# Performance work log

Hardware: AMD Instinct MI355X
Metric: run time of the kernel (lower is better)

## Reference

```python
import jax, jax.numpy as jnp
import numpy as np

# config constants (from init_kwargs)
IMG_W = 800
IMG_H = 320
NUM_POINTS = 72
N_STRIPS = NUM_POINTS - 1
MAX_LANES = 4
REFINE_LAYERS = 3
CLS_W, REG_W, IOU_W = 2.0, 0.5, 2.0
ALPHA_NEG, ALPHA_POS, GAMMA = 0.1, 0.9, 2.0
LIOU_LEN = 15.0


def setup_inputs() -> dict:
    key = jax.random.key(0)
    k1, k2, k3, k4 = jax.random.split(key, 4)
    S, B, N, L, D = REFINE_LAYERS, 32, 2000, MAX_LANES, 2 + 4 + NUM_POINTS
    pred_fir = jax.random.uniform(k1, (S, B, N, D), dtype=jnp.float32)
    pred_sec = jax.random.uniform(k2, (S, B, N, D), dtype=jnp.float32)
    gt = jax.random.uniform(k3, (B, L, D), dtype=jnp.float32)
    gt = gt.at[..., 1].set(1.0)                    # all lanes valid
    # target offsets live in pixel coords; let some fall outside [0, IMG_W) to exercise invalid mask
    gt = gt.at[..., 6:].set(gt[..., 6:] * (IMG_W * 1.1) - 0.05 * IMG_W)
    diff = jax.random.uniform(k4, (S, N), dtype=jnp.float32)
    return {"predictions_fir": pred_fir, "predictions_sec": pred_sec,
            "gt_lane": gt, "diff": diff}


def _greedy_assign(cost):
    # cost: [N, L] -> matched prior row per target column, greedy without replacement
    N = cost.shape[0]
    def body(used, col):
        c = jnp.where(used, jnp.inf, col)
        r = jnp.argmin(c)
        return used.at[r].set(True), r
    _, rows = jax.lax.scan(body, jnp.zeros((N,), bool), cost.T)
    return rows  # [L] int32


def _assign_all(preds, gt):
    # preds: [S,B,N,D], gt: [B,L,D]; matching is under no_grad in the original
    p = jax.lax.stop_gradient(preds)
    t = jax.lax.stop_gradient(gt)
    score = jax.nn.softmax(p[..., :2], axis=-1)[..., 1]            # [S,B,N]
    geo = jnp.abs(p[..., :, None, 2:6] - t[None, :, None, :, 2:6]).sum(-1)   # [S,B,N,L]
    off = jnp.abs(p[..., :, None, 6:] - t[None, :, None, :, 6:] / (IMG_W - 1)).mean(-1)
    cost = geo + off - score[..., None]                            # [S,B,N,L]
    S, B, N, L = cost.shape
    rows = jax.vmap(_greedy_assign)(cost.reshape(S * B, N, L))
    return rows.reshape(S, B, L)


def _smooth_l1(d):
    ad = jnp.abs(d)
    return jnp.where(ad < 1.0, 0.5 * d * d, ad - 0.5)


def _branch_loss(preds, gt):
    # preds: [S,B,N,D], gt: [B,L,D] -> instance loss [N], last matched rows [L]
    S, B, N, _ = preds.shape
    L = gt.shape[1]
    rows = _assign_all(preds, gt)                                  # [S,B,L]

    # focal cls loss, per prior, summed over stages & batch
    cls_t = jax.nn.one_hot(rows, N, dtype=preds.dtype).sum(2)      # [S,B,N] 0/1
    logp = jax.nn.log_softmax(preds[..., :2], axis=-1)
    logpt = jnp.where(cls_t > 0, logp[..., 1], logp[..., 0])
    pt = jnp.exp(logpt)
    alpha_t = jnp.where(cls_t > 0, ALPHA_POS, ALPHA_NEG)
    cls_loss = (-alpha_t * (1.0 - pt) ** GAMMA * logpt).sum((0, 1)) / (B * REFINE_LAYERS)  # [N]

    # gather matched priors: [S,B,L,D]
    pm = jnp.take_along_axis(preds, rows[..., None], axis=2)
    tgt = gt[None]                                                 # [1,B,L,D]

    # smooth-L1 on (y, x, theta, length)
    sc = jnp.array([N_STRIPS, IMG_W - 1, 180.0, N_STRIPS], preds.dtype)
    d = pm[..., 2:6] * sc - tgt[..., 2:6] * sc
    reg_loss = (_smooth_l1(d).mean(-1) / L).sum((0, 1)) / (B * REFINE_LAYERS)  # [L]

    # line IoU loss on offsets
    rp = pm[..., 6:] * (IMG_W - 1)
    rt = jnp.broadcast_to(tgt[..., 6:], rp.shape)
    invalid = (rt < 0) | (rt >= IMG_W)
    ovr = jnp.minimum(rp + LIOU_LEN, rt + LIOU_LEN) - jnp.maximum(rp - LIOU_LEN, rt - LIOU_LEN)
    uni = jnp.maximum(rp + LIOU_LEN, rt + LIOU_LEN) - jnp.minimum(rp - LIOU_LEN, rt - LIOU_LEN)
    ovr = jnp.where(invalid, 0.0, ovr)
    uni = jnp.where(invalid, 0.0, uni)
    iou = ovr.sum(-1) / (uni.sum(-1) + 1e-9)                       # [S,B,L]
    iou_loss = ((1.0 - iou) / L).sum((0, 1)) / (B * REFINE_LAYERS) # [L]

    inst = cls_loss * CLS_W
    rows_last = rows[-1, -1]                                       # last stage, last image
    inst = inst.at[rows_last].add(reg_loss * REG_W + iou_loss * IOU_W)
    return inst


def reference(predictions_fir, predictions_sec, gt_lane, diff):
    loss_A = _branch_loss(predictions_fir, gt_lane)   # [N]
    loss_B = _branch_loss(predictions_sec, gt_lane)   # [N]
    diff_mean = diff.mean(0)                          # [N]
    delta = jax.lax.stop_gradient(jnp.median(loss_A - loss_B))
    loss_A = loss_A - delta / 2
    loss_B = loss_B + delta / 2
    total = jnp.sum((1.0 - diff_mean) * loss_A + diff_mean * loss_B)
    return total
```

## Files before the change

kernel.cpp:

```cpp
#include <hip/hip_runtime.h>
#include <math.h>

#define SDIM 3
#define BDIM 32
#define NPRI 2000
#define LDIM 4
#define DDIM 78
#define NOFF 72
#define NSB (SDIM * BDIM)
#define CHUNK 64
#define NCHUNK 32


__global__ __launch_bounds__(256) void cost_kernel(
    const float* __restrict__ predsA, const float* __restrict__ predsB,
    const float* __restrict__ gt,
    float* __restrict__ costws, float* __restrict__ clsSum)
{
    const int chunk = blockIdx.x;
    const int sb = blockIdx.y;
    const int branch = blockIdx.z;
    const float* preds = branch ? predsB : predsA;
    const int bimg = sb % BDIM;
    const int tid = threadIdx.x;
    const int base_n = chunk * CHUNK;
    const int ntile = min(CHUNK, NPRI - base_n);

    __shared__ float tile[CHUNK * DDIM];
    __shared__ float tg[36 * 8];
    __shared__ float geo4[16];

    {
        const float4* src = (const float4*)(preds + ((size_t)sb * NPRI + base_n) * DDIM);
        const int nf4 = ntile * DDIM / 4;
        for (int k = tid; k < nf4; k += 256) {
            __builtin_amdgcn_global_load_lds(
                (const __attribute__((address_space(1))) unsigned int*)(src + k),
                (__attribute__((address_space(3))) unsigned int*)(&tile[k * 4]),
                16, 0, 0);
        }
    }
    {
        const float* gtb = gt + (size_t)bimg * LDIM * DDIM;
        if (tid < 288) {
            int jj = tid >> 3, t = tid & 7, l = t >> 1, k = t & 1;
            tg[tid] = gtb[l * DDIM + 6 + 2 * jj + k] / 799.0f;
        }
        if (tid < 16) geo4[tid] = gtb[(tid >> 2) * DDIM + 2 + (tid & 3)];
    }
    __syncthreads();

    const int wv = tid >> 6, lane = tid & 63;
    const int il = wv * 16 + (lane >> 2);
    const int h = lane & 3;
    if (il >= ntile) return;
    const int n = base_n + il;
    const float* p = &tile[il * DDIM];

    float offs0 = 0.f, offs1 = 0.f, offs2 = 0.f, offs3 = 0.f;
    const int jj0 = h * 9;
#pragma unroll 3
    for (int jj = jj0; jj < jj0 + 9; ++jj) {
        float pv0 = p[6 + 2 * jj];
        float pv1 = p[7 + 2 * jj];
        const float4* t4 = (const float4*)(tg + jj * 8);
        float4 ta = t4[0], tb = t4[1];
        offs0 += fabsf(pv0 - ta.x); offs0 += fabsf(pv1 - ta.y);
        offs1 += fabsf(pv0 - ta.z); offs1 += fabsf(pv1 - ta.w);
        offs2 += fabsf(pv0 - tb.x); offs2 += fabsf(pv1 - tb.y);
        offs3 += fabsf(pv0 - tb.z); offs3 += fabsf(pv1 - tb.w);
    }
    offs0 += __shfl_xor(offs0, 1); offs1 += __shfl_xor(offs1, 1);
    offs2 += __shfl_xor(offs2, 1); offs3 += __shfl_xor(offs3, 1);
    offs0 += __shfl_xor(offs0, 2); offs1 += __shfl_xor(offs1, 2);
    offs2 += __shfl_xor(offs2, 2); offs3 += __shfl_xor(offs3, 2);

    float a = p[0], b1 = p[1];
    float m = fmaxf(a, b1);
    float ea = expf(a - m), eb = expf(b1 - m);
    float score = eb / (ea + eb);
    float g0 = p[2], g1 = p[3], g2 = p[4], g3 = p[5];

    float mo01 = (h & 1) ? offs1 : offs0;
    float mo23 = (h & 1) ? offs3 : offs2;
    float myoffs = (h & 2) ? mo23 : mo01;

    float geo = fabsf(g0 - geo4[h * 4 + 0]) + fabsf(g1 - geo4[h * 4 + 1])
              + fabsf(g2 - geo4[h * 4 + 2]) + fabsf(g3 - geo4[h * 4 + 3]);
    float* cw = costws + ((size_t)(branch * NSB + sb) * LDIM) * NPRI;
    cw[(size_t)h * NPRI + n] = geo + myoffs / 72.0f - score;

    if (h == 0) {
        float lse = m + logf(ea + eb);
        float logpt = a - lse;
        float pt = expf(logpt);
        float om = 1.0f - pt;
        atomicAdd(&clsSum[branch * NPRI + n], -(0.1f * om * om * logpt));
    }
}

__global__ __launch_bounds__(256) void assignloss_kernel(
    const float* __restrict__ predsA, const float* __restrict__ predsB,
    const float* __restrict__ gt, const float* __restrict__ costws,
    int* __restrict__ rowsws, float* __restrict__ regacc,
    float* __restrict__ corrws)
{
    const int sb = blockIdx.x, branch = blockIdx.y;
    const float* preds = branch ? predsB : predsA;
    const int tid = threadIdx.x;
    const int wv = tid >> 6, lane = tid & 63;
    const int bimg = sb % BDIM;

    __shared__ float cost[LDIM][NPRI];
    __shared__ float redv[4];
    __shared__ int   redi[4];
    __shared__ int   rows_lds[LDIM];

    const float4* src = (const float4*)(costws + (size_t)(branch * NSB + sb) * LDIM * NPRI);
    float4* dst = (float4*)&cost[0][0];
    for (int k = tid; k < LDIM * NPRI / 4; k += 256) dst[k] = src[k];
    __syncthreads();

    for (int l = 0; l < LDIM; ++l) {
        float bv = INFINITY; int bi = 0x7fffffff;
        for (int k = tid; k < NPRI; k += 256) {
            float v = cost[l][k];
            if (v < bv) { bv = v; bi = k; }
        }
#pragma unroll
        for (int off = 32; off > 0; off >>= 1) {
            float v2 = __shfl_down(bv, off);
            int   i2 = __shfl_down(bi, off);
            if (v2 < bv || (v2 == bv && i2 < bi)) { bv = v2; bi = i2; }
        }
        if (lane == 0) { redv[wv] = bv; redi[wv] = bi; }
        __syncthreads();
        if (tid == 0) {
            float fv = redv[0]; int fi = redi[0];
#pragma unroll
            for (int w = 1; w < 4; ++w)
                if (redv[w] < fv || (redv[w] == fv && redi[w] < fi)) { fv = redv[w]; fi = redi[w]; }
            rows_lds[l] = fi;
            cost[0][fi] = INFINITY; cost[1][fi] = INFINITY;
            cost[2][fi] = INFINITY; cost[3][fi] = INFINITY;
        }
        __syncthreads();
    }
    if (tid < LDIM && sb == NSB - 1) rowsws[branch * LDIM + tid] = rows_lds[tid];

    const int l = wv;
    const int row = rows_lds[l];
    const float* pm = preds + ((size_t)sb * NPRI + row) * DDIM;
    const float* tg = gt + ((size_t)bimg * LDIM + l) * DDIM;

    float osum = 0.f, usum = 0.f, rterm = 0.f;
    {
        float rp = pm[6 + lane] * 799.0f;
        float rt = tg[6 + lane];
        bool inv = (rt < 0.0f) || (rt >= 800.0f);
        float ov = fminf(rp, rt) - fmaxf(rp, rt) + 30.0f;
        float un = fmaxf(rp, rt) - fminf(rp, rt) + 30.0f;
        if (!inv) { osum += ov; usum += un; }
    }
    if (lane < 8) {
        float rp = pm[6 + lane + 64] * 799.0f;
        float rt = tg[6 + lane + 64];
        bool inv = (rt < 0.0f) || (rt >= 800.0f);
        float ov = fminf(rp, rt) - fmaxf(rp, rt) + 30.0f;
        float un = fmaxf(rp, rt) - fminf(rp, rt) + 30.0f;
        if (!inv) { osum += ov; usum += un; }
    }
    if (lane < 4) {
        const float scv[4] = {71.0f, 799.0f, 180.0f, 71.0f};
        float s = scv[lane];
        float d = pm[2 + lane] * s - tg[2 + lane] * s;
        float ad = fabsf(d);
        rterm = (ad < 1.0f) ? 0.5f * d * d : ad - 0.5f;
    }
#pragma unroll
    for (int off = 32; off > 0; off >>= 1) {
        osum += __shfl_down(osum, off);
        usum += __shfl_down(usum, off);
        rterm += __shfl_down(rterm, off);
    }
    if (lane == 0) {
        float iou = osum / (usum + 1e-9f);
        atomicAdd(&regacc[branch * 8 + l], (rterm / 4.0f) / 4.0f);
        atomicAdd(&regacc[branch * 8 + 4 + l], (1.0f - iou) / 4.0f);

        float a = pm[0], b1 = pm[1];
        float m = fmaxf(a, b1);
        float ea = expf(a - m), eb = expf(b1 - m);
        float lse = m + logf(ea + eb);
        float lp0 = a - lse, lp1 = b1 - lse;
        float pt0 = expf(lp0), pt1 = expf(lp1);
        float om0 = 1.0f - pt0, om1 = 1.0f - pt1;
        float neg = -(0.1f * om0 * om0 * lp0);
        float pos = -(0.9f * om1 * om1 * lp1);
        atomicAdd(&corrws[branch * NPRI + row], pos - neg);
    }
}

__global__ __launch_bounds__(1024) void final_kernel(
    const float* __restrict__ clsSum, const float* __restrict__ corrws,
    const float* __restrict__ regacc, const int* __restrict__ rowsws,
    const float* __restrict__ diff, float* __restrict__ out)
{
    __shared__ float instA[NPRI];
    __shared__ float instB[NPRI];
    __shared__ float sbuf[2048];
    __shared__ float red[1024];
    const int tid = threadIdx.x;

    for (int n = tid; n < NPRI; n += 1024) {
        float ia = (clsSum[n] + corrws[n]) * (2.0f / 96.0f);
        float ib = (clsSum[NPRI + n] + corrws[NPRI + n]) * (2.0f / 96.0f);
#pragma unroll
        for (int l = 0; l < 4; ++l) {
            if (rowsws[l] == n)
                ia += (regacc[l] / 96.0f) * 0.5f + (regacc[4 + l] / 96.0f) * 2.0f;
            if (rowsws[4 + l] == n)
                ib += (regacc[8 + l] / 96.0f) * 0.5f + (regacc[12 + l] / 96.0f) * 2.0f;
        }
        instA[n] = ia; instB[n] = ib;
        sbuf[n] = ia - ib;
    }
    if (tid < 2048 - NPRI) sbuf[NPRI + tid] = INFINITY;
    __syncthreads();

    for (int k = 2; k <= 2048; k <<= 1) {
        for (int j = k >> 1; j > 0; j >>= 1) {
            for (int i = tid; i < 2048; i += 1024) {
                int ixj = i ^ j;
                if (ixj > i) {
                    bool up = ((i & k) == 0);
                    float x = sbuf[i], y = sbuf[ixj];
                    if ((x > y) == up) { sbuf[i] = y; sbuf[ixj] = x; }
                }
            }
            __syncthreads();
        }
    }
    float delta = 0.5f * (sbuf[999] + sbuf[1000]);

    float acc = 0.0f;
    for (int n = tid; n < NPRI; n += 1024) {
        float dm = (diff[n] + diff[NPRI + n] + diff[2 * NPRI + n]) / 3.0f;
        acc += (1.0f - dm) * (instA[n] - 0.5f * delta)
             + dm * (instB[n] + 0.5f * delta);
    }
    red[tid] = acc;
    __syncthreads();
    for (int s = 512; s > 0; s >>= 1) {
        if (tid < s) red[tid] += red[tid + s];
        __syncthreads();
    }
    if (tid == 0) out[0] = red[0];
}

extern "C" void kernel_launch(void* const* d_in, const int* in_sizes, int n_in,
                              void* d_out, int out_size, void* d_ws, size_t ws_size,
                              hipStream_t stream)
{
    const float* predsA = (const float*)d_in[0];
    const float* predsB = (const float*)d_in[1];
    const float* gt     = (const float*)d_in[2];
    const float* diff   = (const float*)d_in[3];
    float* out = (float*)d_out;

    float* costws = (float*)d_ws;
    int*   rowsws = (int*)(costws + 2 * NSB * LDIM * NPRI);
    float* clsSum = (float*)(rowsws + 8);
    float* corrws = clsSum + 2 * NPRI;
    float* regacc = corrws + 2 * NPRI;

    hipMemsetAsync(clsSum, 0, (4 * NPRI + 16) * sizeof(float), stream);

    dim3 g1(NCHUNK, NSB, 2);
    cost_kernel<<<g1, 256, 0, stream>>>(predsA, predsB, gt, costws, clsSum);

    dim3 g2(NSB, 2);
    assignloss_kernel<<<g2, 256, 0, stream>>>(predsA, predsB, gt, costws,
                                              rowsws, regacc, corrws);

    final_kernel<<<1, 1024, 0, stream>>>(clsSum, corrws, regacc, rowsws, diff, out);
}
```

Measured before the change: 187.0 us.

## Fuse cost computation and greedy assignment into one kernel keeping cost in LDS

Merges the cost kernel and the assignment/loss kernel into a single 1024-thread block per (stage-image, branch). The cost matrix is built directly in shared memory instead of being written to and reread from a global workspace, and one launch is removed. Predictions are now read straight from global memory with per-thread strided float2 loads instead of async LDS staging. Grid parallelism drops from thousands of blocks to 192, which risks underusing the GPU on a bandwidth-bound read.

New measurement: 187.3 us. No clear change (+0.1%).

```diff
diff --git a/kernel.cpp b/kernel.cpp
--- a/kernel.cpp
+++ b/kernel.cpp
@@ -6,40 +6,28 @@
 #define NPRI 2000
 #define LDIM 4
 #define DDIM 78
-#define NOFF 72
 #define NSB (SDIM * BDIM)
-#define CHUNK 64
-#define NCHUNK 32
-
-
-__global__ __launch_bounds__(256) void cost_kernel(
+
+
+__global__ __launch_bounds__(1024) void fused_kernel(
     const float* __restrict__ predsA, const float* __restrict__ predsB,
     const float* __restrict__ gt,
-    float* __restrict__ costws, float* __restrict__ clsSum)
+    int* __restrict__ rowsws, float* __restrict__ regacc,
+    float* __restrict__ corrws, float* __restrict__ clsSum)
 {
-    const int chunk = blockIdx.x;
-    const int sb = blockIdx.y;
-    const int branch = blockIdx.z;
+    const int sb = blockIdx.x, branch = blockIdx.y;
     const float* preds = branch ? predsB : predsA;
     const int bimg = sb % BDIM;
     const int tid = threadIdx.x;
-    const int base_n = chunk * CHUNK;
-    const int ntile = min(CHUNK, NPRI - base_n);
-
-    __shared__ float tile[CHUNK * DDIM];
+    const int wv = tid >> 6, lane = tid & 63;
+
+    __shared__ float cost[LDIM][NPRI];
     __shared__ float tg[36 * 8];
     __shared__ float geo4[16];
-
-    {
-        const float4* src = (const float4*)(preds + ((size_t)sb * NPRI + base_n) * DDIM);
-        const int nf4 = ntile * DDIM / 4;
-        for (int k = tid; k < nf4; k += 256) {
-            __builtin_amdgcn_global_load_lds(
-                (const __attribute__((address_space(1))) unsigned int*)(src + k),
-                (__attribute__((address_space(3))) unsigned int*)(&tile[k * 4]),
-                16, 0, 0);
-        }
-    }
+    __shared__ float redv[16];
+    __shared__ int   redi[16];
+    __shared__ int   rows_lds[LDIM];
+
     {
         const float* gtb = gt + (size_t)bimg * LDIM * DDIM;
         if (tid < 288) {
@@ -50,80 +38,66 @@
     }
     __syncthreads();
 
-    const int wv = tid >> 6, lane = tid & 63;
-    const int il = wv * 16 + (lane >> 2);
-    const int h = lane & 3;
-    if (il >= ntile) return;
-    const int n = base_n + il;
-    const float* p = &tile[il * DDIM];
-
-    float offs0 = 0.f, offs1 = 0.f, offs2 = 0.f, offs3 = 0.f;
-    const int jj0 = h * 9;
-#pragma unroll 3
-    for (int jj = jj0; jj < jj0 + 9; ++jj) {
-        float pv0 = p[6 + 2 * jj];
-        float pv1 = p[7 + 2 * jj];
-        const float4* t4 = (const float4*)(tg + jj * 8);
-        float4 ta = t4[0], tb = t4[1];
-        offs0 += fabsf(pv0 - ta.x); offs0 += fabsf(pv1 - ta.y);
-        offs1 += fabsf(pv0 - ta.z); offs1 += fabsf(pv1 - ta.w);
-        offs2 += fabsf(pv0 - tb.x); offs2 += fabsf(pv1 - tb.y);
-        offs3 += fabsf(pv0 - tb.z); offs3 += fabsf(pv1 - tb.w);
-    }
-    offs0 += __shfl_xor(offs0, 1); offs1 += __shfl_xor(offs1, 1);
-    offs2 += __shfl_xor(offs2, 1); offs3 += __shfl_xor(offs3, 1);
-    offs0 += __shfl_xor(offs0, 2); offs1 += __shfl_xor(offs1, 2);
-    offs2 += __shfl_xor(offs2, 2); offs3 += __shfl_xor(offs3, 2);
-
-    float a = p[0], b1 = p[1];
-    float m = fmaxf(a, b1);
-    float ea = expf(a - m), eb = expf(b1 - m);
-    float score = eb / (ea + eb);
-    float g0 = p[2], g1 = p[3], g2 = p[4], g3 = p[5];
-
-    float mo01 = (h & 1) ? offs1 : offs0;
-    float mo23 = (h & 1) ? offs3 : offs2;
-    float myoffs = (h & 2) ? mo23 : mo01;
-
-    float geo = fabsf(g0 - geo4[h * 4 + 0]) + fabsf(g1 - geo4[h * 4 + 1])
-              + fabsf(g2 - geo4[h * 4 + 2]) + fabsf(g3 - geo4[h * 4 + 3]);
-    float* cw = costws + ((size_t)(branch * NSB + sb) * LDIM) * NPRI;
-    cw[(size_t)h * NPRI + n] = geo + myoffs / 72.0f - score;
-
-    if (h == 0) {
-        float lse = m + logf(ea + eb);
-        float logpt = a - lse;
-        float pt = expf(logpt);
-        float om = 1.0f - pt;
-        atomicAdd(&clsSum[branch * NPRI + n], -(0.1f * om * om * logpt));
-    }
-}
-
-__global__ __launch_bounds__(256) void assignloss_kernel(
-    const float* __restrict__ predsA, const float* __restrict__ predsB,
-    const float* __restrict__ gt, const float* __restrict__ costws,
-    int* __restrict__ rowsws, float* __restrict__ regacc,
-    float* __restrict__ corrws)
-{
-    const int sb = blockIdx.x, branch = blockIdx.y;
-    const float* preds = branch ? predsB : predsA;
-    const int tid = threadIdx.x;
-    const int wv = tid >> 6, lane = tid & 63;
-    const int bimg = sb % BDIM;
-
-    __shared__ float cost[LDIM][NPRI];
-    __shared__ float redv[4];
-    __shared__ int   redi[4];
-    __shared__ int   rows_lds[LDIM];
-
-    const float4* src = (const float4*)(costws + (size_t)(branch * NSB + sb) * LDIM * NPRI);
-    float4* dst = (float4*)&cost[0][0];
-    for (int k = tid; k < LDIM * NPRI / 4; k += 256) dst[k] = src[k];
+    const int h = tid & 3;
+    const float* gpb = preds + (size_t)sb * NPRI * DDIM;
+
+    for (int pass = 0; pass < 8; ++pass) {
+        const int n = pass * 256 + (tid >> 2);
+        if (n < NPRI) {
+            const float* p = gpb + (size_t)n * DDIM;
+            float2 hd0 = *(const float2*)(p);
+            float2 hd1 = *(const float2*)(p + 2);
+            float2 hd2 = *(const float2*)(p + 4);
+            const float2* pb = (const float2*)(p + 6 + h * 18);
+            float2 ov[9];
+#pragma unroll
+            for (int q = 0; q < 9; ++q) ov[q] = pb[q];
+
+            float offs0 = 0.f, offs1 = 0.f, offs2 = 0.f, offs3 = 0.f;
+#pragma unroll
+            for (int q = 0; q < 9; ++q) {
+                float pv0 = ov[q].x;
+                float pv1 = ov[q].y;
+                const float4* t4 = (const float4*)(tg + (h * 9 + q) * 8);
+                float4 ta = t4[0], tb = t4[1];
+                offs0 += fabsf(pv0 - ta.x); offs0 += fabsf(pv1 - ta.y);
+                offs1 += fabsf(pv0 - ta.z); offs1 += fabsf(pv1 - ta.w);
+                offs2 += fabsf(pv0 - tb.x); offs2 += fabsf(pv1 - tb.y);
+                offs3 += fabsf(pv0 - tb.z); offs3 += fabsf(pv1 - tb.w);
+            }
+            offs0 += __shfl_xor(offs0, 1); offs1 += __shfl_xor(offs1, 1);
+            offs2 += __shfl_xor(offs2, 1); offs3 += __shfl_xor(offs3, 1);
+            offs0 += __shfl_xor(offs0, 2); offs1 += __shfl_xor(offs1, 2);
+            offs2 += __shfl_xor(offs2, 2); offs3 += __shfl_xor(offs3, 2);
+
+            float a = hd0.x, b1 = hd0.y;
+            float m = fmaxf(a, b1);
+            float ea = expf(a - m), eb = expf(b1 - m);
+            float score = eb / (ea + eb);
+            float g0 = hd1.x, g1 = hd1.y, g2 = hd2.x, g3 = hd2.y;
+
+            float mo01 = (h & 1) ? offs1 : offs0;
+            float mo23 = (h & 1) ? offs3 : offs2;
+            float myoffs = (h & 2) ? mo23 : mo01;
+
+            float geo = fabsf(g0 - geo4[h * 4 + 0]) + fabsf(g1 - geo4[h * 4 + 1])
+                      + fabsf(g2 - geo4[h * 4 + 2]) + fabsf(g3 - geo4[h * 4 + 3]);
+            cost[h][n] = geo + myoffs / 72.0f - score;
+
+            if (h == 0) {
+                float lse = m + logf(ea + eb);
+                float logpt = a - lse;
+                float pt = expf(logpt);
+                float om = 1.0f - pt;
+                atomicAdd(&clsSum[branch * NPRI + n], -(0.1f * om * om * logpt));
+            }
+        }
+    }
     __syncthreads();
 
     for (int l = 0; l < LDIM; ++l) {
         float bv = INFINITY; int bi = 0x7fffffff;
-        for (int k = tid; k < NPRI; k += 256) {
+        for (int k = tid; k < NPRI; k += 1024) {
             float v = cost[l][k];
             if (v < bv) { bv = v; bi = k; }
         }
@@ -138,7 +112,7 @@
         if (tid == 0) {
             float fv = redv[0]; int fi = redi[0];
 #pragma unroll
-            for (int w = 1; w < 4; ++w)
+            for (int w = 1; w < 16; ++w)
                 if (redv[w] < fv || (redv[w] == fv && redi[w] < fi)) { fv = redv[w]; fi = redi[w]; }
             rows_lds[l] = fi;
             cost[0][fi] = INFINITY; cost[1][fi] = INFINITY;
@@ -148,56 +122,58 @@
     }
     if (tid < LDIM && sb == NSB - 1) rowsws[branch * LDIM + tid] = rows_lds[tid];
 
-    const int l = wv;
-    const int row = rows_lds[l];
-    const float* pm = preds + ((size_t)sb * NPRI + row) * DDIM;
-    const float* tg = gt + ((size_t)bimg * LDIM + l) * DDIM;
-
-    float osum = 0.f, usum = 0.f, rterm = 0.f;
-    {
-        float rp = pm[6 + lane] * 799.0f;
-        float rt = tg[6 + lane];
-        bool inv = (rt < 0.0f) || (rt >= 800.0f);
-        float ov = fminf(rp, rt) - fmaxf(rp, rt) + 30.0f;
-        float un = fmaxf(rp, rt) - fminf(rp, rt) + 30.0f;
-        if (!inv) { osum += ov; usum += un; }
-    }
-    if (lane < 8) {
-        float rp = pm[6 + lane + 64] * 799.0f;
-        float rt = tg[6 + lane + 64];
-        bool inv = (rt < 0.0f) || (rt >= 800.0f);
-        float ov = fminf(rp, rt) - fmaxf(rp, rt) + 30.0f;
-        float un = fmaxf(rp, rt) - fminf(rp, rt) + 30.0f;
-        if (!inv) { osum += ov; usum += un; }
-    }
-    if (lane < 4) {
-        const float scv[4] = {71.0f, 799.0f, 180.0f, 71.0f};
-        float s = scv[lane];
-        float d = pm[2 + lane] * s - tg[2 + lane] * s;
-        float ad = fabsf(d);
-        rterm = (ad < 1.0f) ? 0.5f * d * d : ad - 0.5f;
-    }
-#pragma unroll
-    for (int off = 32; off > 0; off >>= 1) {
-        osum += __shfl_down(osum, off);
-        usum += __shfl_down(usum, off);
-        rterm += __shfl_down(rterm, off);
-    }
-    if (lane == 0) {
-        float iou = osum / (usum + 1e-9f);
-        atomicAdd(&regacc[branch * 8 + l], (rterm / 4.0f) / 4.0f);
-        atomicAdd(&regacc[branch * 8 + 4 + l], (1.0f - iou) / 4.0f);
-
-        float a = pm[0], b1 = pm[1];
-        float m = fmaxf(a, b1);
-        float ea = expf(a - m), eb = expf(b1 - m);
-        float lse = m + logf(ea + eb);
-        float lp0 = a - lse, lp1 = b1 - lse;
-        float pt0 = expf(lp0), pt1 = expf(lp1);
-        float om0 = 1.0f - pt0, om1 = 1.0f - pt1;
-        float neg = -(0.1f * om0 * om0 * lp0);
-        float pos = -(0.9f * om1 * om1 * lp1);
-        atomicAdd(&corrws[branch * NPRI + row], pos - neg);
+    if (wv < 4) {
+        const int l = wv;
+        const int row = rows_lds[l];
+        const float* pm = preds + ((size_t)sb * NPRI + row) * DDIM;
+        const float* tgp = gt + ((size_t)bimg * LDIM + l) * DDIM;
+
+        float osum = 0.f, usum = 0.f, rterm = 0.f;
+        {
+            float rp = pm[6 + lane] * 799.0f;
+            float rt = tgp[6 + lane];
+            bool inv = (rt < 0.0f) || (rt >= 800.0f);
+            float ov = fminf(rp, rt) - fmaxf(rp, rt) + 30.0f;
+            float un = fmaxf(rp, rt) - fminf(rp, rt) + 30.0f;
+            if (!inv) { osum += ov; usum += un; }
+        }
+        if (lane < 8) {
+            float rp = pm[6 + lane + 64] * 799.0f;
+            float rt = tgp[6 + lane + 64];
+            bool inv = (rt < 0.0f) || (rt >= 800.0f);
+            float ov = fminf(rp, rt) - fmaxf(rp, rt) + 30.0f;
+            float un = fmaxf(rp, rt) - fminf(rp, rt) + 30.0f;
+            if (!inv) { osum += ov; usum += un; }
+        }
+        if (lane < 4) {
+            const float scv[4] = {71.0f, 799.0f, 180.0f, 71.0f};
+            float s = scv[lane];
+            float d = pm[2 + lane] * s - tgp[2 + lane] * s;
+            float ad = fabsf(d);
+            rterm = (ad < 1.0f) ? 0.5f * d * d : ad - 0.5f;
+        }
+#pragma unroll
+        for (int off = 32; off > 0; off >>= 1) {
+            osum += __shfl_down(osum, off);
+            usum += __shfl_down(usum, off);
+            rterm += __shfl_down(rterm, off);
+        }
+        if (lane == 0) {
+            float iou = osum / (usum + 1e-9f);
+            atomicAdd(&regacc[branch * 8 + l], (rterm / 4.0f) / 4.0f);
+            atomicAdd(&regacc[branch * 8 + 4 + l], (1.0f - iou) / 4.0f);
+
+            float a = pm[0], b1 = pm[1];
+            float m = fmaxf(a, b1);
+            float ea = expf(a - m), eb = expf(b1 - m);
+            float lse = m + logf(ea + eb);
+            float lp0 = a - lse, lp1 = b1 - lse;
+            float pt0 = expf(lp0), pt1 = expf(lp1);
+            float om0 = 1.0f - pt0, om1 = 1.0f - pt1;
+            float neg = -(0.1f * om0 * om0 * lp0);
+            float pos = -(0.9f * om1 * om1 * lp1);
+            atomicAdd(&corrws[branch * NPRI + row], pos - neg);
+        }
     }
 }
 
@@ -268,20 +244,16 @@
     const float* diff   = (const float*)d_in[3];
     float* out = (float*)d_out;
 
-    float* costws = (float*)d_ws;
-    int*   rowsws = (int*)(costws + 2 * NSB * LDIM * NPRI);
+    int*   rowsws = (int*)d_ws;
     float* clsSum = (float*)(rowsws + 8);
     float* corrws = clsSum + 2 * NPRI;
     float* regacc = corrws + 2 * NPRI;
 
     hipMemsetAsync(clsSum, 0, (4 * NPRI + 16) * sizeof(float), stream);
 
-    dim3 g1(NCHUNK, NSB, 2);
-    cost_kernel<<<g1, 256, 0, stream>>>(predsA, predsB, gt, costws, clsSum);
-
-    dim3 g2(NSB, 2);
-    assignloss_kernel<<<g2, 256, 0, stream>>>(predsA, predsB, gt, costws,
-                                              rowsws, regacc, corrws);
+    dim3 g1(NSB, 2);
+    fused_kernel<<<g1, 1024, 0, stream>>>(predsA, predsB, gt,
+                                          rowsws, regacc, corrws, clsSum);
 
     final_kernel<<<1, 1024, 0, stream>>>(clsSum, corrws, regacc, rowsws, diff, out);
 }
```
